# Kernel tuning notes

Measured on AMD Instinct MI355X. Metric: run time of the kernel, lower is better.

## Reference

```python
import jax, jax.numpy as jnp
import numpy as np

N_NODES = 100000
N_EDGES = 1_600_000
D = 64
E_POS = 20000
NEG = 100


def setup_inputs() -> dict:
    key = jax.random.key(0)
    ks = jax.random.split(key, 10)
    s = 1.0 / np.sqrt(D)
    return {
        "features": jax.random.normal(ks[0], (N_NODES, D), dtype=jnp.float32),
        "W1": jax.random.normal(ks[1], (D, D), dtype=jnp.float32) * s,
        "b1": jnp.zeros((D,), dtype=jnp.float32),
        "W2": jax.random.normal(ks[2], (D, D), dtype=jnp.float32) * s,
        "b2": jnp.zeros((D,), dtype=jnp.float32),
        "src": jax.random.randint(ks[3], (N_EDGES,), 0, N_NODES, dtype=jnp.int32),
        "dst": jax.random.randint(ks[4], (N_EDGES,), 0, N_NODES, dtype=jnp.int32),
        "pos_src": jax.random.randint(ks[5], (E_POS,), 0, N_NODES, dtype=jnp.int32),
        "pos_dst": jax.random.randint(ks[6], (E_POS,), 0, N_NODES, dtype=jnp.int32),
        "neg_src": jax.random.randint(ks[7], (E_POS * NEG,), 0, N_NODES, dtype=jnp.int32),
        "neg_dst": jax.random.randint(ks[8], (E_POS * NEG,), 0, N_NODES, dtype=jnp.int32),
        "neg_sample_size": NEG,
    }


def _sage_gcn(h, src, dst, W, b, n):
    # DGL SAGEConv 'gcn' aggregator: (sum of in-neighbor feats + self) / (in_deg + 1), then Linear
    neigh = jax.ops.segment_sum(h[src], dst, num_segments=n)           # [N, D]
    deg = jax.ops.segment_sum(jnp.ones((src.shape[0],), h.dtype), dst, num_segments=n)
    h_neigh = (neigh + h) / (deg[:, None] + 1.0)
    return h_neigh @ W + b


def reference(features, W1, b1, W2, b2, src, dst, pos_src, pos_dst, neg_src, neg_dst, neg_sample_size):
    n = features.shape[0]
    h = jax.nn.relu(_sage_gcn(features, src, dst, W1, b1, n))
    emb = _sage_gcn(h, src, dst, W2, b2, n)                            # [N, D]
    pos_score = jnp.sum(emb[pos_src] * emb[pos_dst], axis=1)           # [E_pos]
    neg_score = jnp.sum(emb[neg_src] * emb[neg_dst], axis=1)           # [E_pos*NEG]
    pos_ls = jax.nn.log_sigmoid(pos_score)
    neg_ls = jax.nn.log_sigmoid(-neg_score).reshape(-1, neg_sample_size)
    return jnp.mean(-pos_ls - jnp.sum(neg_ls, axis=1))
```

## Files before the change

kernel.cpp:

```cpp
#include <hip/hip_runtime.h>
#include <hip/hip_fp16.h>
#include <math.h>

#define D 64
#define NPB 64
#define NPB_SHIFT 6
#define LCAP 2560
#define NPART 256
#define NV 2

typedef _Float16 half4v __attribute__((ext_vector_type(4)));
typedef float f32x4 __attribute__((ext_vector_type(4)));


__global__ void scan1_kernel(const int* __restrict__ in, int* __restrict__ out,
                             int* __restrict__ bsum, int n) {
    __shared__ int s[1024];
    int t = threadIdx.x;
    int i = blockIdx.x * 1024 + t;
    int v = (i < n) ? in[i] : 0;
    s[t] = v;
    __syncthreads();
    for (int off = 1; off < 1024; off <<= 1) {
        int add = (t >= off) ? s[t - off] : 0;
        __syncthreads();
        s[t] += add;
        __syncthreads();
    }
    if (i < n) out[i] = s[t] - v;
    if (t == 1023) bsum[blockIdx.x] = s[1023];
}

__global__ void scan2_kernel(int* __restrict__ bsum, int nb) {
    __shared__ int s[1024];
    int t = threadIdx.x;
    int v = (t < nb) ? bsum[t] : 0;
    s[t] = v;
    __syncthreads();
    for (int off = 1; off < 1024; off <<= 1) {
        int add = (t >= off) ? s[t - off] : 0;
        __syncthreads();
        s[t] += add;
        __syncthreads();
    }
    if (t < nb) bsum[t] = s[t] - v;
}

__global__ void scan3_kernel(int* __restrict__ out, const int* __restrict__ bsum, int n) {
    int i = blockIdx.x * 1024 + threadIdx.x;
    if (i < n) out[i] += bsum[blockIdx.x];
}


__global__ __launch_bounds__(256) void part_hist_kernel(
    const int* __restrict__ dst, int* __restrict__ harr,
    int e, int nb, int chunk)
{
    extern __shared__ int sh[];
    const int p = blockIdx.x;
    for (int i = threadIdx.x; i < nb; i += 256) sh[i] = 0;
    __syncthreads();
    const int s = p * chunk, ee = min(e, s + chunk);
    for (int i = s + threadIdx.x; i < ee; i += 256)
        atomicAdd(&sh[dst[i] >> NPB_SHIFT], 1);
    __syncthreads();
    for (int b = threadIdx.x; b < nb; b += 256) harr[b * NPART + p] = sh[b];
}

__global__ __launch_bounds__(256) void part_scatter_kernel(
    const int* __restrict__ src, const int* __restrict__ dst,
    const int* __restrict__ soff, int* __restrict__ packed,
    int e, int nb, int chunk)
{
    extern __shared__ int cur[];
    const int p = blockIdx.x;
    for (int b = threadIdx.x; b < nb; b += 256) cur[b] = soff[b * NPART + p];
    __syncthreads();
    const int s = p * chunk, ee = min(e, s + chunk);
    for (int i = s + threadIdx.x; i < ee; i += 256) {
        int d = dst[i];
        int pos = atomicAdd(&cur[d >> NPB_SHIFT], 1);
        packed[pos] = src[i] | ((d & (NPB - 1)) << 24);
    }
}

__global__ __launch_bounds__(256) void bucket_build_kernel(
    const int* __restrict__ soff, const int* __restrict__ packed,
    int* __restrict__ csr, int* __restrict__ rs,
    int n, int e_total, int nb)
{
    __shared__ int lcsr[LCAP];
    __shared__ int dcount[NPB];
    __shared__ int dexcl[NPB];
    __shared__ int cur2[NPB];
    const int b    = blockIdx.x;
    const int base = soff[b * NPART];
    const int end  = (b + 1 < nb) ? soff[(b + 1) * NPART] : e_total;
    const int cnt  = end - base;
    const int nb0  = b << NPB_SHIFT;
    const int nnode = min(NPB, n - nb0);
    const int tid  = threadIdx.x;

    if (tid < NPB) { dcount[tid] = 0; cur2[tid] = 0; }
    __syncthreads();

    for (int i = tid; i < cnt; i += 256)
        atomicAdd(&dcount[(packed[base + i] >> 24) & (NPB - 1)], 1);
    __syncthreads();
    if (tid == 0) {
        int run = 0;
        for (int t = 0; t < nnode; ++t) { dexcl[t] = run; run += dcount[t]; }
    }
    __syncthreads();
    if (tid < nnode) rs[nb0 + tid] = base + dexcl[tid];

    if (cnt <= LCAP) {
        for (int i = tid; i < cnt; i += 256) {
            int pk = packed[base + i];
            int ln = (pk >> 24) & (NPB - 1);
            int pos = dexcl[ln] + atomicAdd(&cur2[ln], 1);
            lcsr[pos] = pk & 0xFFFFFF;
        }
        __syncthreads();
        for (int i = tid; i < cnt; i += 256) csr[base + i] = lcsr[i];
    } else {
        for (int i = tid; i < cnt; i += 256) {
            int pk = packed[base + i];
            int ln = (pk >> 24) & (NPB - 1);
            int pos = dexcl[ln] + atomicAdd(&cur2[ln], 1);
            csr[base + pos] = pk & 0xFFFFFF;
        }
    }
}


__global__ __launch_bounds__(256) void f2h_kernel(const float* __restrict__ in,
                                                  __half* __restrict__ out, int n4) {
    int i = blockIdx.x * blockDim.x + threadIdx.x;
    if (i < n4) {
        float4 v = *(const float4*)(in + (size_t)i * 4);
        union { __half2 h[2]; float2 f; } u;
        u.h[0] = __floats2half2_rn(v.x, v.y);
        u.h[1] = __floats2half2_rn(v.z, v.w);
        *(float2*)(out + (size_t)i * 4) = u.f;
    }
}


__device__ __forceinline__ void unpack8(float4 f, float* x) {
    __half2* h = reinterpret_cast<__half2*>(&f);
    #pragma unroll
    for (int i = 0; i < 4; ++i) {
        float2 t = __half22float2(h[i]);
        x[2 * i] = t.x; x[2 * i + 1] = t.y;
    }
}

__global__ __launch_bounds__(256) void agg_kernel(
    const __half* __restrict__ in, const int* __restrict__ csr,
    const int* __restrict__ rs, __half* __restrict__ anorm,
    int n, int e_total)
{
    const int ll = threadIdx.x & 7;
    const int g  = (blockIdx.x * 256 + threadIdx.x) >> 3;
    const int v0 = g * NV;
    if (v0 >= n) return;

    #pragma unroll
    for (int t = 0; t < NV; ++t) {
        const int v = v0 + t;
        if (v >= n) break;
        const int i0 = rs[v];
        const int i1 = (v + 1 < n) ? rs[v + 1] : e_total;
        const int m  = i1 - i0;

        float acc[8];
        #pragma unroll
        for (int j = 0; j < 8; ++j) acc[j] = 0.0f;

        float4 f0, f1;
        if (m > 0) f0 = *(const float4*)(in + (size_t)csr[i0] * D + ll * 8);
        if (m > 1) f1 = *(const float4*)(in + (size_t)csr[i0 + 1] * D + ll * 8);
        for (int i = 0; i < m; ++i) {
            float4 fn;
            if (i + 2 < m) fn = *(const float4*)(in + (size_t)csr[i0 + i + 2] * D + ll * 8);
            float x[8]; unpack8(f0, x);
            #pragma unroll
            for (int j = 0; j < 8; ++j) acc[j] += x[j];
            f0 = f1; f1 = fn;
        }

        float4 sf = *(const float4*)(in + (size_t)v * D + ll * 8);
        float sx[8]; unpack8(sf, sx);
        const float inv = 1.0f / (float)(m + 1);
        union { __half h[8]; float4 f; } u;
        #pragma unroll
        for (int j = 0; j < 8; ++j) u.h[j] = __float2half((acc[j] + sx[j]) * inv);
        *(float4*)(anorm + (size_t)v * D + ll * 8) = u.f;
    }
}


template<int RELU>
__global__ __launch_bounds__(256) void post_mfma_kernel(
    const __half* __restrict__ anorm, __half* __restrict__ out,
    const float* __restrict__ W, const float* __restrict__ bias, int n)
{
    const int lane = threadIdx.x & 63;
    const int w    = threadIdx.x >> 6;
    const int tile = blockIdx.x * 4 + w;
    const int v0   = tile * 16;
    if (v0 >= n) return;

    const int col = lane & 15;
    const int kb  = (lane >> 4) * 4;

    half4v bf[4][4];
    #pragma unroll
    for (int kt = 0; kt < 4; ++kt)
        #pragma unroll
        for (int t = 0; t < 4; ++t)
            #pragma unroll
            for (int j = 0; j < 4; ++j)
                bf[kt][t][j] = (_Float16)W[(kt * 16 + kb + j) * D + t * 16 + col];

    int vr = v0 + col; if (vr >= n) vr = n - 1;
    const __half* ap = anorm + (size_t)vr * D + kb;
    half4v af[4];
    #pragma unroll
    for (int kt = 0; kt < 4; ++kt)
        af[kt] = *(const half4v*)(ap + kt * 16);

    f32x4 c[4];
    #pragma unroll
    for (int t = 0; t < 4; ++t) {
        float bv = bias[t * 16 + col];
        c[t] = (f32x4){bv, bv, bv, bv};
    }
    #pragma unroll
    for (int kt = 0; kt < 4; ++kt)
        #pragma unroll
        for (int t = 0; t < 4; ++t)
            c[t] = __builtin_amdgcn_mfma_f32_16x16x16f16(af[kt], bf[kt][t], c[t], 0, 0, 0);

    #pragma unroll
    for (int t = 0; t < 4; ++t)
        #pragma unroll
        for (int p = 0; p < 4; ++p) {
            int r = v0 + (lane >> 4) * 4 + p;
            if (r < n) {
                float o = c[t][p];
                if (RELU) o = fmaxf(o, 0.0f);
                out[(size_t)r * D + t * 16 + col] = __float2half(o);
            }
        }
}


__global__ __launch_bounds__(256) void score_kernel(
    const __half* __restrict__ emb,
    const int* __restrict__ a_idx, const int* __restrict__ b_idx,
    int npairs, float sign, double* __restrict__ accum)
{
    const int ll  = threadIdx.x & 7;
    const int gib = threadIdx.x >> 3;
    const int gpb = blockDim.x >> 3;
    int g = blockIdx.x * gpb + gib;
    const int stride = gridDim.x * gpb;

    float local = 0.0f;
    int p = g;
    for (; p + stride < npairs; p += 2 * stride) {
        int p2 = p + stride;
        int ai = a_idx[p],  bi = b_idx[p];
        int ci = a_idx[p2], di = b_idx[p2];
        float4 fa = *(const float4*)(emb + (size_t)ai * D + ll * 8);
        float4 fb = *(const float4*)(emb + (size_t)bi * D + ll * 8);
        float4 fc = *(const float4*)(emb + (size_t)ci * D + ll * 8);
        float4 fd = *(const float4*)(emb + (size_t)di * D + ll * 8);
        float A[8], B[8], C[8], E[8];
        unpack8(fa, A); unpack8(fb, B); unpack8(fc, C); unpack8(fd, E);
        float d0 = 0.f, d1 = 0.f;
        #pragma unroll
        for (int j = 0; j < 8; ++j) { d0 = fmaf(A[j], B[j], d0); d1 = fmaf(C[j], E[j], d1); }
        d0 += __shfl_xor(d0, 1); d1 += __shfl_xor(d1, 1);
        d0 += __shfl_xor(d0, 2); d1 += __shfl_xor(d1, 2);
        d0 += __shfl_xor(d0, 4); d1 += __shfl_xor(d1, 4);
        if (ll == 0) {
            float x0 = sign * d0, x1 = sign * d1;
            local += fmaxf(x0, 0.0f) + log1pf(expf(-fabsf(x0)));
            local += fmaxf(x1, 0.0f) + log1pf(expf(-fabsf(x1)));
        }
    }
    for (; p < npairs; p += stride) {
        int ai = a_idx[p], bi = b_idx[p];
        float4 fa = *(const float4*)(emb + (size_t)ai * D + ll * 8);
        float4 fb = *(const float4*)(emb + (size_t)bi * D + ll * 8);
        float A[8], B[8];
        unpack8(fa, A); unpack8(fb, B);
        float d = 0.f;
        #pragma unroll
        for (int j = 0; j < 8; ++j) d = fmaf(A[j], B[j], d);
        d += __shfl_xor(d, 1);
        d += __shfl_xor(d, 2);
        d += __shfl_xor(d, 4);
        if (ll == 0) {
            float x = sign * d;
            local += fmaxf(x, 0.0f) + log1pf(expf(-fabsf(x)));
        }
    }

    __shared__ float red[256];
    red[threadIdx.x] = local;
    __syncthreads();
    for (int s = blockDim.x / 2; s > 0; s >>= 1) {
        if ((int)threadIdx.x < s) red[threadIdx.x] += red[threadIdx.x + s];
        __syncthreads();
    }
    if (threadIdx.x == 0) atomicAdd(accum, (double)red[0]);
}

__global__ void finalize_kernel(const double* __restrict__ acc, float* __restrict__ out, int ep) {
    if (threadIdx.x == 0 && blockIdx.x == 0)
        out[0] = (float)(acc[0] / (double)ep);
}


extern "C" void kernel_launch(void* const* d_in, const int* in_sizes, int n_in,
                              void* d_out, int out_size, void* d_ws, size_t ws_size,
                              hipStream_t stream) {
    const float* features = (const float*)d_in[0];
    const float* W1 = (const float*)d_in[1];
    const float* b1 = (const float*)d_in[2];
    const float* W2 = (const float*)d_in[3];
    const float* b2 = (const float*)d_in[4];
    const int* src     = (const int*)d_in[5];
    const int* dst     = (const int*)d_in[6];
    const int* pos_src = (const int*)d_in[7];
    const int* pos_dst = (const int*)d_in[8];
    const int* neg_src = (const int*)d_in[9];
    const int* neg_dst = (const int*)d_in[10];

    const int N    = in_sizes[0] / D;
    const int E    = in_sizes[5];
    const int EP   = in_sizes[7];
    const int ENEG = in_sizes[9];
    const int NB   = (N + NPB - 1) >> NPB_SHIFT;

    char* ws = (char*)d_ws;
    size_t off = 0;
    auto alloc = [&](size_t bytes) -> void* {
        void* p = ws + off;
        off += (bytes + 255) & ~(size_t)255;
        return p;
    };
    int*    rs     = (int*)alloc((size_t)(N + 64) * 4);
    int*    harr   = (int*)alloc((size_t)NB * NPART * 4);
    int*    soff   = (int*)alloc((size_t)NB * NPART * 4);
    int*    bsum   = (int*)alloc(1024 * 4);
    int*    packed = (int*)alloc((size_t)E * 4);
    int*    csr    = (int*)alloc((size_t)E * 4);
    __half* anorm  = (__half*)alloc((size_t)N * D * 2);
    __half* featH  = (__half*)alloc((size_t)N * D * 2);
    __half* hH     = (__half*)alloc((size_t)N * D * 2);
    __half* embH   = (__half*)alloc((size_t)N * D * 2);
    double* acc    = (double*)alloc(8);

    hipMemsetAsync(acc, 0, 8, stream);

    const int chunk = (E + NPART - 1) / NPART;
    const size_t ldsNB = (size_t)NB * 4;

    part_hist_kernel<<<NPART, 256, ldsNB, stream>>>(dst, harr, E, NB, chunk);
    const int scn = NB * NPART;
    const int nbs = (scn + 1023) / 1024;
    scan1_kernel<<<nbs, 1024, 0, stream>>>(harr, soff, bsum, scn);
    scan2_kernel<<<1, 1024, 0, stream>>>(bsum, nbs);
    scan3_kernel<<<nbs, 1024, 0, stream>>>(soff, bsum, scn);
    part_scatter_kernel<<<NPART, 256, ldsNB, stream>>>(src, dst, soff, packed, E, NB, chunk);
    bucket_build_kernel<<<NB, 256, 0, stream>>>(soff, packed, csr, rs, N, E, NB);

    const int n4 = (N * D) / 4;
    f2h_kernel<<<(n4 + 255) / 256, 256, 0, stream>>>(features, featH, n4);

    const int ngroups = (N + NV - 1) / NV;
    const int ab = (ngroups * 8 + 255) / 256;
    const int ntiles = (N + 15) / 16;
    const int pb2 = (ntiles + 3) / 4;

    agg_kernel<<<ab, 256, 0, stream>>>(featH, csr, rs, anorm, N, E);
    post_mfma_kernel<1><<<pb2, 256, 0, stream>>>(anorm, hH, W1, b1, N);

    agg_kernel<<<ab, 256, 0, stream>>>(hH, csr, rs, anorm, N, E);
    post_mfma_kernel<0><<<pb2, 256, 0, stream>>>(anorm, embH, W2, b2, N);

    int pb = (EP + 31) / 32;  if (pb > 2048) pb = 2048;
    score_kernel<<<pb, 256, 0, stream>>>(embH, pos_src, pos_dst, EP, -1.0f, acc);
    int ngb = (ENEG + 31) / 32; if (ngb > 4096) ngb = 4096;
    score_kernel<<<ngb, 256, 0, stream>>>(embH, neg_src, neg_dst, ENEG, 1.0f, acc);

    finalize_kernel<<<1, 64, 0, stream>>>(acc, (float*)d_out, EP);
}
```

Before: 261.0 us.

## Store embeddings as fp8 and compute pair scores with fp8 MFMA diagonals

The second layer's output is written as fp8 bytes instead of fp16, halving the embedding size read by the score kernels. The score kernel is rewritten so that each wave handles 16 pairs per tile and computes their dot products with two fp8 16x16x32 MFMA instructions, keeping only the diagonal entries. This targets the memory traffic of the 2M random gathers. The cost is much lower precision in the embeddings and in the loss, plus wasted off-diagonal MFMA work.

```diff
diff --git a/kernel.cpp b/kernel.cpp
--- a/kernel.cpp
+++ b/kernel.cpp
@@ -201,9 +201,10 @@
 }
 
 
-template<int RELU>
+template<int RELU, int FP8OUT>
 __global__ __launch_bounds__(256) void post_mfma_kernel(
-    const __half* __restrict__ anorm, __half* __restrict__ out,
+    const __half* __restrict__ anorm, __half* __restrict__ outh,
+    unsigned char* __restrict__ out8,
     const float* __restrict__ W, const float* __restrict__ bias, int n)
 {
     const int lane = threadIdx.x & 63;
@@ -251,61 +252,85 @@
             if (r < n) {
                 float o = c[t][p];
                 if (RELU) o = fmaxf(o, 0.0f);
-                out[(size_t)r * D + t * 16 + col] = __float2half(o);
+                if (FP8OUT) {
+                    int pk = __builtin_amdgcn_cvt_pk_fp8_f32(o, o, 0, false);
+                    out8[(size_t)r * D + t * 16 + col] = (unsigned char)(pk & 0xFF);
+                } else {
+                    outh[(size_t)r * D + t * 16 + col] = __float2half(o);
+                }
             }
         }
 }
 
 
-__global__ __launch_bounds__(256) void score_kernel(
-    const __half* __restrict__ emb,
+__global__ __launch_bounds__(256) void score_mfma_kernel(
+    const unsigned char* __restrict__ emb8,
     const int* __restrict__ a_idx, const int* __restrict__ b_idx,
     int npairs, float sign, double* __restrict__ accum)
 {
-    const int ll  = threadIdx.x & 7;
-    const int gib = threadIdx.x >> 3;
-    const int gpb = blockDim.x >> 3;
-    int g = blockIdx.x * gpb + gib;
-    const int stride = gridDim.x * gpb;
+    const int lane = threadIdx.x & 63;
+    const int gw   = (blockIdx.x * blockDim.x + threadIdx.x) >> 6;
+    const int nw   = (gridDim.x * blockDim.x) >> 6;
+    const int ntiles = (npairs + 15) >> 4;
+
+    const int pr = lane & 15;
+    const int ks = lane >> 4;
+    const bool has = (ks == (pr >> 2));
+    const int reg  = pr & 3;
 
     float local = 0.0f;
-    int p = g;
-    for (; p + stride < npairs; p += 2 * stride) {
-        int p2 = p + stride;
-        int ai = a_idx[p],  bi = b_idx[p];
-        int ci = a_idx[p2], di = b_idx[p2];
-        float4 fa = *(const float4*)(emb + (size_t)ai * D + ll * 8);
-        float4 fb = *(const float4*)(emb + (size_t)bi * D + ll * 8);
-        float4 fc = *(const float4*)(emb + (size_t)ci * D + ll * 8);
-        float4 fd = *(const float4*)(emb + (size_t)di * D + ll * 8);
-        float A[8], B[8], C[8], E[8];
-        unpack8(fa, A); unpack8(fb, B); unpack8(fc, C); unpack8(fd, E);
-        float d0 = 0.f, d1 = 0.f;
-        #pragma unroll
-        for (int j = 0; j < 8; ++j) { d0 = fmaf(A[j], B[j], d0); d1 = fmaf(C[j], E[j], d1); }
-        d0 += __shfl_xor(d0, 1); d1 += __shfl_xor(d1, 1);
-        d0 += __shfl_xor(d0, 2); d1 += __shfl_xor(d1, 2);
-        d0 += __shfl_xor(d0, 4); d1 += __shfl_xor(d1, 4);
-        if (ll == 0) {
-            float x0 = sign * d0, x1 = sign * d1;
-            local += fmaxf(x0, 0.0f) + log1pf(expf(-fabsf(x0)));
-            local += fmaxf(x1, 0.0f) + log1pf(expf(-fabsf(x1)));
-        }
-    }
-    for (; p < npairs; p += stride) {
-        int ai = a_idx[p], bi = b_idx[p];
-        float4 fa = *(const float4*)(emb + (size_t)ai * D + ll * 8);
-        float4 fb = *(const float4*)(emb + (size_t)bi * D + ll * 8);
-        float A[8], B[8];
-        unpack8(fa, A); unpack8(fb, B);
-        float d = 0.f;
-        #pragma unroll
-        for (int j = 0; j < 8; ++j) d = fmaf(A[j], B[j], d);
-        d += __shfl_xor(d, 1);
-        d += __shfl_xor(d, 2);
-        d += __shfl_xor(d, 4);
-        if (ll == 0) {
-            float x = sign * d;
+
+    int t = gw;
+    for (; t + nw < ntiles; t += 2 * nw) {
+        int t2 = t + nw;
+        int p0 = t * 16 + pr, p1 = t2 * 16 + pr;
+        int c0 = min(p0, npairs - 1), c1 = min(p1, npairs - 1);
+        int ia0 = a_idx[c0], ib0 = b_idx[c0];
+        int ia1 = a_idx[c1], ib1 = b_idx[c1];
+        const unsigned char* pa0 = emb8 + ((size_t)ia0 << 6) + ks * 8;
+        const unsigned char* pb0 = emb8 + ((size_t)ib0 << 6) + ks * 8;
+        const unsigned char* pa1 = emb8 + ((size_t)ia1 << 6) + ks * 8;
+        const unsigned char* pb1 = emb8 + ((size_t)ib1 << 6) + ks * 8;
+        long a00 = *(const long*)pa0;
+        long a01 = *(const long*)(pa0 + 32);
+        long b00 = *(const long*)pb0;
+        long b01 = *(const long*)(pb0 + 32);
+        long a10 = *(const long*)pa1;
+        long a11 = *(const long*)(pa1 + 32);
+        long b10 = *(const long*)pb1;
+        long b11 = *(const long*)(pb1 + 32);
+        f32x4 c0v = {0.f, 0.f, 0.f, 0.f};
+        f32x4 c1v = {0.f, 0.f, 0.f, 0.f};
+        c0v = __builtin_amdgcn_mfma_f32_16x16x32_fp8_fp8(a00, b00, c0v, 0, 0, 0);
+        c0v = __builtin_amdgcn_mfma_f32_16x16x32_fp8_fp8(a01, b01, c0v, 0, 0, 0);
+        c1v = __builtin_amdgcn_mfma_f32_16x16x32_fp8_fp8(a10, b10, c1v, 0, 0, 0);
+        c1v = __builtin_amdgcn_mfma_f32_16x16x32_fp8_fp8(a11, b11, c1v, 0, 0, 0);
+        if (has) {
+            if (p0 < npairs) {
+                float x = sign * c0v[reg];
+                local += fmaxf(x, 0.0f) + log1pf(expf(-fabsf(x)));
+            }
+            if (p1 < npairs) {
+                float x = sign * c1v[reg];
+                local += fmaxf(x, 0.0f) + log1pf(expf(-fabsf(x)));
+            }
+        }
+    }
+    for (; t < ntiles; t += nw) {
+        int p0 = t * 16 + pr;
+        int c0 = min(p0, npairs - 1);
+        int ia = a_idx[c0], ib = b_idx[c0];
+        const unsigned char* pa = emb8 + ((size_t)ia << 6) + ks * 8;
+        const unsigned char* pb = emb8 + ((size_t)ib << 6) + ks * 8;
+        long a0 = *(const long*)pa;
+        long a1 = *(const long*)(pa + 32);
+        long b0 = *(const long*)pb;
+        long b1 = *(const long*)(pb + 32);
+        f32x4 cv = {0.f, 0.f, 0.f, 0.f};
+        cv = __builtin_amdgcn_mfma_f32_16x16x32_fp8_fp8(a0, b0, cv, 0, 0, 0);
+        cv = __builtin_amdgcn_mfma_f32_16x16x32_fp8_fp8(a1, b1, cv, 0, 0, 0);
+        if (has && p0 < npairs) {
+            float x = sign * cv[reg];
             local += fmaxf(x, 0.0f) + log1pf(expf(-fabsf(x)));
         }
     }
@@ -363,7 +388,7 @@
     __half* anorm  = (__half*)alloc((size_t)N * D * 2);
     __half* featH  = (__half*)alloc((size_t)N * D * 2);
     __half* hH     = (__half*)alloc((size_t)N * D * 2);
-    __half* embH   = (__half*)alloc((size_t)N * D * 2);
+    unsigned char* emb8 = (unsigned char*)alloc((size_t)N * D);
     double* acc    = (double*)alloc(8);
 
     hipMemsetAsync(acc, 0, 8, stream);
@@ -385,19 +410,19 @@
 
     const int ngroups = (N + NV - 1) / NV;
     const int ab = (ngroups * 8 + 255) / 256;
-    const int ntiles = (N + 15) / 16;
-    const int pb2 = (ntiles + 3) / 4;
+    const int ntiles16 = (N + 15) / 16;
+    const int pb2 = (ntiles16 + 3) / 4;
 
     agg_kernel<<<ab, 256, 0, stream>>>(featH, csr, rs, anorm, N, E);
-    post_mfma_kernel<1><<<pb2, 256, 0, stream>>>(anorm, hH, W1, b1, N);
+    post_mfma_kernel<1, 0><<<pb2, 256, 0, stream>>>(anorm, hH, nullptr, W1, b1, N);
 
     agg_kernel<<<ab, 256, 0, stream>>>(hH, csr, rs, anorm, N, E);
-    post_mfma_kernel<0><<<pb2, 256, 0, stream>>>(anorm, embH, W2, b2, N);
-
-    int pb = (EP + 31) / 32;  if (pb > 2048) pb = 2048;
-    score_kernel<<<pb, 256, 0, stream>>>(embH, pos_src, pos_dst, EP, -1.0f, acc);
-    int ngb = (ENEG + 31) / 32; if (ngb > 4096) ngb = 4096;
-    score_kernel<<<ngb, 256, 0, stream>>>(embH, neg_src, neg_dst, ENEG, 1.0f, acc);
+    post_mfma_kernel<0, 1><<<pb2, 256, 0, stream>>>(anorm, nullptr, emb8, W2, b2, N);
+
+    int pb = ((EP + 15) / 16 + 3) / 4;  if (pb > 2048) pb = 2048; if (pb < 1) pb = 1;
+    score_mfma_kernel<<<pb, 256, 0, stream>>>(emb8, pos_src, pos_dst, EP, -1.0f, acc);
+    int ngb = ((ENEG + 15) / 16 + 3) / 4; if (ngb > 1024) ngb = 1024;
+    score_mfma_kernel<<<ngb, 256, 0, stream>>>(emb8, neg_src, neg_dst, ENEG, 1.0f, acc);
 
     finalize_kernel<<<1, 64, 0, stream>>>(acc, (float*)d_out, EP);
 }
```

Result: faster. 235.7 us (-9.7%).
